# Kernel tuning notes

Hardware: AMD Instinct MI355X
Metric: run time of the kernel (lower is better)

## Reference

```python
import jax, jax.numpy as jnp
import numpy as np

IN_CH = 2048
OUT_CH = 2048
BATCH = 8192


def setup_inputs() -> dict:
    key = jax.random.key(0)
    ks = jax.random.split(key, 8)
    bound = 1.0 / np.sqrt(IN_CH)  # torch nn.Linear default init range
    inp = {
        "input": jax.random.normal(ks[0], (BATCH, IN_CH), dtype=jnp.float32),
        "hidden": jax.random.normal(ks[1], (BATCH, OUT_CH), dtype=jnp.float32),
        "cell": jax.random.normal(ks[2], (BATCH, OUT_CH), dtype=jnp.float32),
        # Fused gate weights: [IN_CH, 4*OUT_CH] for (forget, input, output, state)
        "W": jax.random.uniform(ks[3], (IN_CH, 4 * OUT_CH), minval=-bound, maxval=bound, dtype=jnp.float32),
        "b": jax.random.uniform(ks[4], (4 * OUT_CH,), minval=-bound, maxval=bound, dtype=jnp.float32),
    }
    return inp


def reference(input, hidden, cell, W, b):
    # One fused GEMM for all four gates, then fused elementwise gate math.
    gates = input @ W + b  # [B, 4*OUT_CH]
    f_g, i_g, o_g, s_g = jnp.split(gates, 4, axis=-1)
    # NOTE: original module applies sigmoid (not tanh) to the state gate.
    forget_gate = jax.nn.sigmoid(f_g)
    input_gate = jax.nn.sigmoid(i_g)
    output_gate = jax.nn.sigmoid(o_g)
    state_gate = jax.nn.sigmoid(s_g)
    new_cell = forget_gate * cell + input_gate * state_gate
    new_hidden = output_gate * jnp.tanh(new_cell)
    return (new_hidden, new_cell)
```

## Files before the change

kernel.cpp:

```cpp
#include <hip/hip_runtime.h>
#include <cstddef>
#include <cstdint>

#define B_ROWS 8192
#define K_DIM  2048
#define N_GATE 2048
#define NG     4
#define W_COLS (NG * N_GATE)

#define BM  128
#define BGN 64
#define BK  32
#define KT  (K_DIM / BK)

typedef __attribute__((ext_vector_type(8))) short s16x8;
typedef __attribute__((ext_vector_type(4))) short s16x4;
typedef __attribute__((ext_vector_type(4))) float f32x4;

__device__ __forceinline__ float fast_sigmoid(float x) {
  return 1.0f / (1.0f + __expf(-x));
}
__device__ __forceinline__ float fast_tanh(float x) {
  return 1.0f - 2.0f / (__expf(2.0f * x) + 1.0f);
}

__global__ void convert_in_kernel(const float4* __restrict__ src,
                                  s16x4* __restrict__ dst, int n4) {
  int idx = blockIdx.x * blockDim.x + threadIdx.x;
  int stride = gridDim.x * blockDim.x;
  for (int i = idx; i < n4; i += stride) {
    float4 v = src[i];
    s16x4 o = { __builtin_bit_cast(short, (__bf16)v.x),
                __builtin_bit_cast(short, (__bf16)v.y),
                __builtin_bit_cast(short, (__bf16)v.z),
                __builtin_bit_cast(short, (__bf16)v.w) };
    dst[i] = o;
  }
}

__global__ void convert_w_kernel(const float* __restrict__ W,
                                 short* __restrict__ Wt) {
  __shared__ float tile[32][33];
  int n0 = blockIdx.x * 32;
  int k0 = blockIdx.y * 32;
  int tx = threadIdx.x, ty = threadIdx.y;
#pragma unroll
  for (int j = 0; j < 32; j += 8)
    tile[ty + j][tx] = W[(size_t)(k0 + ty + j) * W_COLS + n0 + tx];
  __syncthreads();
#pragma unroll
  for (int j = 0; j < 32; j += 8)
    Wt[(size_t)(n0 + ty + j) * K_DIM + k0 + tx] =
        __builtin_bit_cast(short, (__bf16)tile[tx][ty + j]);
}

#define GL16(gsrc, ldst)                                                        \
  __builtin_amdgcn_global_load_lds(                                             \
      (const __attribute__((address_space(1))) unsigned int*)(gsrc),            \
      (__attribute__((address_space(3))) unsigned int*)(ldst), 16, 0, 0)

__global__ __launch_bounds__(256, 2) void lstm_gemm_kernel(
    const short* __restrict__ Abf,
    const short* __restrict__ Wt,
    const float* __restrict__ bias,
    const float* __restrict__ cell,
    float* __restrict__ outH,
    float* __restrict__ outC) {
  __shared__ short As[2][BM * BK];
  __shared__ short Bs[2][NG * BGN * BK];

  const int tid = threadIdx.x;
  const int lane = tid & 63;
  const int wid = tid >> 6;
  const int wm = wid >> 1;
  const int wn = wid & 1;
  const int lrow = lane & 15;
  const int lk = lane >> 4;

  const int bid = blockIdx.x;
  const int x = bid & 7;
  const int ii = bid >> 3;
  const int tn = x * 4 + (ii & 3);
  const int tm = ii >> 2;
  const int m0 = tm * BM;
  const int n0 = tn * BGN;

  f32x4 acc[NG][4][2];
#pragma unroll
  for (int g = 0; g < NG; ++g)
#pragma unroll
    for (int mi = 0; mi < 4; ++mi)
#pragma unroll
      for (int ni = 0; ni < 2; ++ni)
        acc[g][mi][ni] = (f32x4){0.f, 0.f, 0.f, 0.f};

  int a_off[4];
#pragma unroll
  for (int mi = 0; mi < 4; ++mi) {
    int ar = wm * 64 + mi * 16 + lrow;
    a_off[mi] = (ar * 4 + (lk ^ ((ar >> 1) & 3))) * 16;
  }
  int b_off[NG][2];
#pragma unroll
  for (int g = 0; g < NG; ++g)
#pragma unroll
    for (int ni = 0; ni < 2; ++ni) {
      int br = wn * 32 + ni * 16 + lrow;
      b_off[g][ni] = (g * 256 + br * 4 + (lk ^ ((br >> 1) & 3))) * 16;
    }

  auto stage = [&](int buf, int kk) {
#pragma unroll
    for (int j = 0; j < 2; ++j) {
      int p = j * 256 + tid;
      int row = p >> 2;
      int gl = (p & 3) ^ ((p >> 3) & 3);
      GL16(Abf + (size_t)(m0 + row) * K_DIM + kk + gl * 8, &As[buf][p * 8]);
    }
#pragma unroll
    for (int g = 0; g < NG; ++g) {
      int row = tid >> 2;
      int gl = (tid & 3) ^ ((tid >> 3) & 3);
      GL16(Wt + (size_t)(g * N_GATE + n0 + row) * K_DIM + kk + gl * 8,
           &Bs[buf][(g * 256 + tid) * 8]);
    }
  };

  stage(0, 0);
  __syncthreads();

  for (int kt = 0; kt < KT; ++kt) {
    const int cur = kt & 1;
    if (kt + 1 < KT) stage(cur ^ 1, (kt + 1) * BK);

    const char* abase = (const char*)As[cur];
    const char* bbase = (const char*)Bs[cur];
    s16x8 af[4];
#pragma unroll
    for (int mi = 0; mi < 4; ++mi)
      af[mi] = *reinterpret_cast<const s16x8*>(abase + a_off[mi]);
#pragma unroll
    for (int g = 0; g < NG; ++g) {
      s16x8 bf0 = *reinterpret_cast<const s16x8*>(bbase + b_off[g][0]);
      s16x8 bf1 = *reinterpret_cast<const s16x8*>(bbase + b_off[g][1]);
#pragma unroll
      for (int mi = 0; mi < 4; ++mi) {
        acc[g][mi][0] = __builtin_amdgcn_mfma_f32_16x16x32_bf16(
            af[mi], bf0, acc[g][mi][0], 0, 0, 0);
        acc[g][mi][1] = __builtin_amdgcn_mfma_f32_16x16x32_bf16(
            af[mi], bf1, acc[g][mi][1], 0, 0, 0);
      }
    }
    __syncthreads();
  }

#pragma unroll
  for (int ni = 0; ni < 2; ++ni) {
    const int n = n0 + wn * 32 + ni * 16 + lrow;
    const float bf_ = bias[n];
    const float bi_ = bias[N_GATE + n];
    const float bo_ = bias[2 * N_GATE + n];
    const float bs_ = bias[3 * N_GATE + n];
#pragma unroll
    for (int mi = 0; mi < 4; ++mi) {
#pragma unroll
      for (int r = 0; r < 4; ++r) {
        const int m = m0 + wm * 64 + mi * 16 + lk * 4 + r;
        const size_t off = (size_t)m * N_GATE + n;
        const float fg = fast_sigmoid(acc[0][mi][ni][r] + bf_);
        const float ig = fast_sigmoid(acc[1][mi][ni][r] + bi_);
        const float og = fast_sigmoid(acc[2][mi][ni][r] + bo_);
        const float sg = fast_sigmoid(acc[3][mi][ni][r] + bs_);
        const float cn = fg * cell[off] + ig * sg;
        outC[off] = cn;
        outH[off] = og * fast_tanh(cn);
      }
    }
  }
}

extern "C" void kernel_launch(void* const* d_in, const int* in_sizes, int n_in,
                              void* d_out, int out_size, void* d_ws, size_t ws_size,
                              hipStream_t stream) {
  const float* inp  = (const float*)d_in[0];
  const float* cell = (const float*)d_in[2];
  const float* W    = (const float*)d_in[3];
  const float* bias = (const float*)d_in[4];

  float* outH = (float*)d_out;
  float* outC = (float*)d_out + (size_t)B_ROWS * N_GATE;

  short* Abf = (short*)d_ws;
  short* Wt  = (short*)d_ws + (size_t)B_ROWS * K_DIM;

  {
    int n4 = (B_ROWS * K_DIM) / 4;
    convert_in_kernel<<<2048, 256, 0, stream>>>((const float4*)inp,
                                                (s16x4*)Abf, n4);
  }
  {
    dim3 grid(W_COLS / 32, K_DIM / 32);
    dim3 block(32, 8);
    convert_w_kernel<<<grid, block, 0, stream>>>(W, Wt);
  }
  {
    int nblocks = (B_ROWS / BM) * (N_GATE / BGN);
    lstm_gemm_kernel<<<nblocks, 256, 0, stream>>>(Abf, Wt, bias, cell,
                                                  outH, outC);
  }
}
```

Before: 609.5 us.

## Rewrite LSTM GEMM with 256x256 tiles, 8 waves, phased staging pipeline

The fused-gate GEMM moves to a 256-row by 64-column-per-gate block with 512 threads and BK=64. It uses 128KB of dynamic LDS with XOR-swizzled layouts and an explicit phased schedule that interleaves global-to-LDS staging with MFMA bursts, using manual vmcnt waits, barriers and setprio. The input conversion now handles 8 elements per thread, and the weight transpose kernel uses 64x64 tiles with packed bf16 pairs and 16-byte stores. The aim is more data reuse per block and better overlap of loads with compute, at the cost of a large LDS footprint, higher register pressure and fragile hand-written synchronisation.

```diff
diff --git a/kernel.cpp b/kernel.cpp
--- a/kernel.cpp
+++ b/kernel.cpp
@@ -8,13 +8,11 @@
 #define NG     4
 #define W_COLS (NG * N_GATE)
 
-#define BM  128
-#define BGN 64
-#define BK  32
-#define KT  (K_DIM / BK)
+#define BM   256
+#define BK   64
+#define NTIL 32
 
 typedef __attribute__((ext_vector_type(8))) short s16x8;
-typedef __attribute__((ext_vector_type(4))) short s16x4;
 typedef __attribute__((ext_vector_type(4))) float f32x4;
 
 __device__ __forceinline__ float fast_sigmoid(float x) {
@@ -25,33 +23,66 @@
 }
 
 __global__ void convert_in_kernel(const float4* __restrict__ src,
-                                  s16x4* __restrict__ dst, int n4) {
+                                  s16x8* __restrict__ dst, int n8) {
   int idx = blockIdx.x * blockDim.x + threadIdx.x;
   int stride = gridDim.x * blockDim.x;
-  for (int i = idx; i < n4; i += stride) {
-    float4 v = src[i];
-    s16x4 o = { __builtin_bit_cast(short, (__bf16)v.x),
-                __builtin_bit_cast(short, (__bf16)v.y),
-                __builtin_bit_cast(short, (__bf16)v.z),
-                __builtin_bit_cast(short, (__bf16)v.w) };
+  for (int i = idx; i < n8; i += stride) {
+    float4 a = src[2 * i], b = src[2 * i + 1];
+    s16x8 o = { __builtin_bit_cast(short, (__bf16)a.x),
+                __builtin_bit_cast(short, (__bf16)a.y),
+                __builtin_bit_cast(short, (__bf16)a.z),
+                __builtin_bit_cast(short, (__bf16)a.w),
+                __builtin_bit_cast(short, (__bf16)b.x),
+                __builtin_bit_cast(short, (__bf16)b.y),
+                __builtin_bit_cast(short, (__bf16)b.z),
+                __builtin_bit_cast(short, (__bf16)b.w) };
     dst[i] = o;
   }
 }
 
-__global__ void convert_w_kernel(const float* __restrict__ W,
-                                 short* __restrict__ Wt) {
-  __shared__ float tile[32][33];
-  int n0 = blockIdx.x * 32;
-  int k0 = blockIdx.y * 32;
-  int tx = threadIdx.x, ty = threadIdx.y;
-#pragma unroll
-  for (int j = 0; j < 32; j += 8)
-    tile[ty + j][tx] = W[(size_t)(k0 + ty + j) * W_COLS + n0 + tx];
+__device__ __forceinline__ unsigned int pack2bf16(float x, float y) {
+  unsigned short lo = __builtin_bit_cast(unsigned short, (__bf16)x);
+  unsigned short hi = __builtin_bit_cast(unsigned short, (__bf16)y);
+  return ((unsigned int)hi << 16) | lo;
+}
+
+__global__ __launch_bounds__(256) void convert_w_kernel(const float* __restrict__ W,
+                                                        short* __restrict__ Wt) {
+  __shared__ unsigned int tile[64 * 32];
+  const int t = threadIdx.x;
+  const int n0 = blockIdx.x * 64;
+  const int k0 = blockIdx.y * 64;
+  {
+    const int kr = t >> 2, seg = t & 3;
+    const float4* src = (const float4*)(W + (size_t)(k0 + kr) * W_COLS + n0 + seg * 16);
+#pragma unroll
+    for (int u = 0; u < 4; ++u) {
+      float4 v = src[u];
+      const int np = seg * 8 + u * 2;
+      tile[kr * 32 + (np ^ (kr & 31))]       = pack2bf16(v.x, v.y);
+      tile[kr * 32 + ((np + 1) ^ (kr & 31))] = pack2bf16(v.z, v.w);
+    }
+  }
   __syncthreads();
-#pragma unroll
-  for (int j = 0; j < 32; j += 8)
-    Wt[(size_t)(n0 + ty + j) * K_DIM + k0 + tx] =
-        __builtin_bit_cast(short, (__bf16)tile[tx][ty + j]);
+  {
+    const int np = t >> 3;
+    const int kb = t & 7;
+    unsigned int w[8];
+#pragma unroll
+    for (int v = 0; v < 8; ++v) {
+      const int k = kb * 8 + v;
+      w[v] = tile[k * 32 + (np ^ (k & 31))];
+    }
+    s16x8 lo, hi;
+#pragma unroll
+    for (int v = 0; v < 8; ++v) {
+      lo[v] = (short)(w[v] & 0xffff);
+      hi[v] = (short)(w[v] >> 16);
+    }
+    short* d0 = Wt + (size_t)(n0 + 2 * np) * K_DIM + k0 + kb * 8;
+    *(s16x8*)d0 = lo;
+    *(s16x8*)(d0 + K_DIM) = hi;
+  }
 }
 
 #define GL16(gsrc, ldst)                                                        \
@@ -59,118 +90,152 @@
       (const __attribute__((address_space(1))) unsigned int*)(gsrc),            \
       (__attribute__((address_space(3))) unsigned int*)(ldst), 16, 0, 0)
 
-__global__ __launch_bounds__(256, 2) void lstm_gemm_kernel(
+#define MFMA16 __builtin_amdgcn_mfma_f32_16x16x32_bf16
+
+__global__ __launch_bounds__(512, 2) void lstm_gemm_kernel(
     const short* __restrict__ Abf,
     const short* __restrict__ Wt,
     const float* __restrict__ bias,
     const float* __restrict__ cell,
     float* __restrict__ outH,
     float* __restrict__ outC) {
-  __shared__ short As[2][BM * BK];
-  __shared__ short Bs[2][NG * BGN * BK];
+  extern __shared__ short lds[];
 
   const int tid = threadIdx.x;
   const int lane = tid & 63;
   const int wid = tid >> 6;
-  const int wm = wid >> 1;
-  const int wn = wid & 1;
+  const int wm = wid >> 2;
+  const int wn = wid & 3;
   const int lrow = lane & 15;
   const int lk = lane >> 4;
 
   const int bid = blockIdx.x;
-  const int x = bid & 7;
-  const int ii = bid >> 3;
-  const int tn = x * 4 + (ii & 3);
-  const int tm = ii >> 2;
+  const int xcd = bid & 7, j = bid >> 3;
+  const int tn = xcd * 4 + (j >> 5);
+  const int tm = j & 31;
   const int m0 = tm * BM;
-  const int n0 = tn * BGN;
-
-  f32x4 acc[NG][4][2];
-#pragma unroll
-  for (int g = 0; g < NG; ++g)
-#pragma unroll
-    for (int mi = 0; mi < 4; ++mi)
-#pragma unroll
-      for (int ni = 0; ni < 2; ++ni)
-        acc[g][mi][ni] = (f32x4){0.f, 0.f, 0.f, 0.f};
-
-  int a_off[4];
-#pragma unroll
-  for (int mi = 0; mi < 4; ++mi) {
-    int ar = wm * 64 + mi * 16 + lrow;
-    a_off[mi] = (ar * 4 + (lk ^ ((ar >> 1) & 3))) * 16;
-  }
-  int b_off[NG][2];
-#pragma unroll
-  for (int g = 0; g < NG; ++g)
-#pragma unroll
-    for (int ni = 0; ni < 2; ++ni) {
-      int br = wn * 32 + ni * 16 + lrow;
-      b_off[g][ni] = (g * 256 + br * 4 + (lk ^ ((br >> 1) & 3))) * 16;
-    }
-
-  auto stage = [&](int buf, int kk) {
-#pragma unroll
-    for (int j = 0; j < 2; ++j) {
-      int p = j * 256 + tid;
-      int row = p >> 2;
-      int gl = (p & 3) ^ ((p >> 3) & 3);
-      GL16(Abf + (size_t)(m0 + row) * K_DIM + kk + gl * 8, &As[buf][p * 8]);
-    }
-#pragma unroll
-    for (int g = 0; g < NG; ++g) {
-      int row = tid >> 2;
-      int gl = (tid & 3) ^ ((tid >> 3) & 3);
-      GL16(Wt + (size_t)(g * N_GATE + n0 + row) * K_DIM + kk + gl * 8,
-           &Bs[buf][(g * 256 + tid) * 8]);
-    }
-  };
-
-  stage(0, 0);
-  __syncthreads();
-
-  for (int kt = 0; kt < KT; ++kt) {
-    const int cur = kt & 1;
-    if (kt + 1 < KT) stage(cur ^ 1, (kt + 1) * BK);
-
-    const char* abase = (const char*)As[cur];
-    const char* bbase = (const char*)Bs[cur];
-    s16x8 af[4];
-#pragma unroll
-    for (int mi = 0; mi < 4; ++mi)
-      af[mi] = *reinterpret_cast<const s16x8*>(abase + a_off[mi]);
-#pragma unroll
-    for (int g = 0; g < NG; ++g) {
-      s16x8 bf0 = *reinterpret_cast<const s16x8*>(bbase + b_off[g][0]);
-      s16x8 bf1 = *reinterpret_cast<const s16x8*>(bbase + b_off[g][1]);
-#pragma unroll
-      for (int mi = 0; mi < 4; ++mi) {
-        acc[g][mi][0] = __builtin_amdgcn_mfma_f32_16x16x32_bf16(
-            af[mi], bf0, acc[g][mi][0], 0, 0, 0);
-        acc[g][mi][1] = __builtin_amdgcn_mfma_f32_16x16x32_bf16(
-            af[mi], bf1, acc[g][mi][1], 0, 0, 0);
-      }
-    }
-    __syncthreads();
-  }
-
-#pragma unroll
-  for (int ni = 0; ni < 2; ++ni) {
-    const int n = n0 + wn * 32 + ni * 16 + lrow;
-    const float bf_ = bias[n];
-    const float bi_ = bias[N_GATE + n];
-    const float bo_ = bias[2 * N_GATE + n];
-    const float bs_ = bias[3 * N_GATE + n];
-#pragma unroll
-    for (int mi = 0; mi < 4; ++mi) {
+  const int n0 = tn * 64;
+
+  size_t a_src[2][2], b_src[2][2];
+#pragma unroll
+  for (int h = 0; h < 2; ++h)
+#pragma unroll
+    for (int jj = 0; jj < 2; ++jj) {
+      const int p = h * 1024 + jj * 512 + tid;
+      const int r = p >> 3;
+      const int gl = (p & 7) ^ (r & 7);
+      a_src[h][jj] = (size_t)(m0 + r) * K_DIM + gl * 8;
+      const int wn16 = r >> 6, g = (r >> 4) & 3, nc4 = r & 15;
+      b_src[h][jj] = (size_t)(g * N_GATE + n0 + wn16 * 16 + nc4) * K_DIM + gl * 8;
+    }
+
+#define STAGE_A(BUF, H, KT) do {                                                 \
+    GL16(Abf + a_src[H][0] + (size_t)(KT) * BK,                                  \
+         lds + (BUF) * 16384 + ((H) * 1024 + tid) * 8);                          \
+    GL16(Abf + a_src[H][1] + (size_t)(KT) * BK,                                  \
+         lds + (BUF) * 16384 + ((H) * 1024 + 512 + tid) * 8);                    \
+  } while (0)
+#define STAGE_B(BUF, H, KT) do {                                                 \
+    GL16(Wt + b_src[H][0] + (size_t)(KT) * BK,                                   \
+         lds + 32768 + (BUF) * 16384 + ((H) * 1024 + tid) * 8);                  \
+    GL16(Wt + b_src[H][1] + (size_t)(KT) * BK,                                   \
+         lds + 32768 + (BUF) * 16384 + ((H) * 1024 + 512 + tid) * 8);            \
+  } while (0)
+
+  const int pg0 = (lk ^ (lrow & 7)) * 16;
+  const int pg1 = ((4 + lk) ^ (lrow & 7)) * 16;
+  const char* aK0 = (const char*)lds + (wm * 128 + lrow) * 128 + pg0;
+  const char* aK1 = (const char*)lds + (wm * 128 + lrow) * 128 + pg1;
+  const char* bK0 = (const char*)lds + 65536 + (wn * 64 + lrow) * 128 + pg0;
+  const char* bK1 = (const char*)lds + 65536 + (wn * 64 + lrow) * 128 + pg1;
+#define AF(BUF, MI, KK) (*(const s16x8*)(aK##KK + (BUF) * 32768 + (MI) * 2048))
+#define BFR(BUF, G, KK) (*(const s16x8*)(bK##KK + (BUF) * 32768 + (G) * 2048))
+
+  f32x4 acc[8][4];
+#pragma unroll
+  for (int mi = 0; mi < 8; ++mi)
+#pragma unroll
+    for (int g = 0; g < 4; ++g) acc[mi][g] = (f32x4){0.f, 0.f, 0.f, 0.f};
+
+  s16x8 bfr[4][2];
+
+#define MMQ(MI, A0, A1) do {                                                     \
+    acc[MI][0] = MFMA16(A0, bfr[0][0], acc[MI][0], 0, 0, 0);                     \
+    acc[MI][0] = MFMA16(A1, bfr[0][1], acc[MI][0], 0, 0, 0);                     \
+    acc[MI][1] = MFMA16(A0, bfr[1][0], acc[MI][1], 0, 0, 0);                     \
+    acc[MI][1] = MFMA16(A1, bfr[1][1], acc[MI][1], 0, 0, 0);                     \
+    acc[MI][2] = MFMA16(A0, bfr[2][0], acc[MI][2], 0, 0, 0);                     \
+    acc[MI][2] = MFMA16(A1, bfr[2][1], acc[MI][2], 0, 0, 0);                     \
+    acc[MI][3] = MFMA16(A0, bfr[3][0], acc[MI][3], 0, 0, 0);                     \
+    acc[MI][3] = MFMA16(A1, bfr[3][1], acc[MI][3], 0, 0, 0);                     \
+  } while (0)
+
+#define VM_NONE do {} while (0)
+#define VM_4 asm volatile("s_waitcnt vmcnt(4)" ::: "memory")
+#define VM_0 asm volatile("s_waitcnt vmcnt(0)" ::: "memory")
+
+#define PHASE(BUF, Q, LOADB, STG, VM) do {                                       \
+    if (LOADB) {                                                                 \
+      bfr[0][0] = BFR(BUF, 0, 0); bfr[0][1] = BFR(BUF, 0, 1);                    \
+      bfr[1][0] = BFR(BUF, 1, 0); bfr[1][1] = BFR(BUF, 1, 1);                    \
+      bfr[2][0] = BFR(BUF, 2, 0); bfr[2][1] = BFR(BUF, 2, 1);                    \
+      bfr[3][0] = BFR(BUF, 3, 0); bfr[3][1] = BFR(BUF, 3, 1);                    \
+    }                                                                            \
+    s16x8 af00 = AF(BUF, 2 * (Q), 0), af01 = AF(BUF, 2 * (Q), 1);                \
+    s16x8 af10 = AF(BUF, 2 * (Q) + 1, 0), af11 = AF(BUF, 2 * (Q) + 1, 1);        \
+    STG;                                                                         \
+    VM;                                                                          \
+    __builtin_amdgcn_s_barrier();                                                \
+    asm volatile("s_waitcnt lgkmcnt(0)" ::: "memory");                           \
+    __builtin_amdgcn_s_setprio(1);                                               \
+    MMQ(2 * (Q), af00, af01);                                                    \
+    MMQ(2 * (Q) + 1, af10, af11);                                                \
+    __builtin_amdgcn_s_setprio(0);                                               \
+    __builtin_amdgcn_s_barrier();                                                \
+  } while (0)
+
+  STAGE_B(0, 0, 0); STAGE_B(0, 1, 0); STAGE_A(0, 0, 0); STAGE_A(0, 1, 0);
+  STAGE_B(1, 0, 1); STAGE_B(1, 1, 1);
+  VM_4;
+  __builtin_amdgcn_s_barrier();
+
+  for (int i = 0; i < NTIL / 2 - 1; ++i) {
+    const int t1 = 2 * i + 1, t2 = 2 * i + 2, t3 = 2 * i + 3;
+    PHASE(0, 0, 1, { STAGE_A(1, 0, t1); }, VM_NONE);
+    PHASE(0, 1, 0, { STAGE_A(1, 1, t1); }, VM_NONE);
+    PHASE(0, 2, 0, { STAGE_B(0, 0, t2); }, VM_NONE);
+    PHASE(0, 3, 0, { STAGE_B(0, 1, t2); }, VM_4);
+    PHASE(1, 0, 1, { STAGE_A(0, 0, t2); }, VM_NONE);
+    PHASE(1, 1, 0, { STAGE_A(0, 1, t2); }, VM_NONE);
+    PHASE(1, 2, 0, { STAGE_B(1, 0, t3); }, VM_NONE);
+    PHASE(1, 3, 0, { STAGE_B(1, 1, t3); }, VM_4);
+  }
+
+  PHASE(0, 0, 1, { STAGE_A(1, 0, 31); }, VM_NONE);
+  PHASE(0, 1, 0, { STAGE_A(1, 1, 31); }, VM_NONE);
+  PHASE(0, 2, 0, {}, VM_NONE);
+  PHASE(0, 3, 0, {}, VM_0);
+  PHASE(1, 0, 1, {}, VM_NONE);
+  PHASE(1, 1, 0, {}, VM_NONE);
+  PHASE(1, 2, 0, {}, VM_NONE);
+  PHASE(1, 3, 0, {}, VM_NONE);
+
+  {
+    const int n = n0 + wn * 16 + lrow;
+    const float b0 = bias[n];
+    const float b1 = bias[N_GATE + n];
+    const float b2 = bias[2 * N_GATE + n];
+    const float b3 = bias[3 * N_GATE + n];
+    const size_t base = (size_t)(m0 + wm * 128 + lk * 4) * N_GATE + n;
+#pragma unroll
+    for (int mi = 0; mi < 8; ++mi) {
 #pragma unroll
       for (int r = 0; r < 4; ++r) {
-        const int m = m0 + wm * 64 + mi * 16 + lk * 4 + r;
-        const size_t off = (size_t)m * N_GATE + n;
-        const float fg = fast_sigmoid(acc[0][mi][ni][r] + bf_);
-        const float ig = fast_sigmoid(acc[1][mi][ni][r] + bi_);
-        const float og = fast_sigmoid(acc[2][mi][ni][r] + bo_);
-        const float sg = fast_sigmoid(acc[3][mi][ni][r] + bs_);
+        const size_t off = base + (size_t)(mi * 16 + r) * N_GATE;
+        const float fg = fast_sigmoid(acc[mi][0][r] + b0);
+        const float ig = fast_sigmoid(acc[mi][1][r] + b1);
+        const float og = fast_sigmoid(acc[mi][2][r] + b2);
+        const float sg = fast_sigmoid(acc[mi][3][r] + b3);
         const float cn = fg * cell[off] + ig * sg;
         outC[off] = cn;
         outH[off] = og * fast_tanh(cn);
@@ -194,18 +259,19 @@
   short* Wt  = (short*)d_ws + (size_t)B_ROWS * K_DIM;
 
   {
-    int n4 = (B_ROWS * K_DIM) / 4;
+    int n8 = (B_ROWS * K_DIM) / 8;
     convert_in_kernel<<<2048, 256, 0, stream>>>((const float4*)inp,
-                                                (s16x4*)Abf, n4);
-  }
-  {
-    dim3 grid(W_COLS / 32, K_DIM / 32);
-    dim3 block(32, 8);
-    convert_w_kernel<<<grid, block, 0, stream>>>(W, Wt);
-  }
-  {
-    int nblocks = (B_ROWS / BM) * (N_GATE / BGN);
-    lstm_gemm_kernel<<<nblocks, 256, 0, stream>>>(Abf, Wt, bias, cell,
-                                                  outH, outC);
-  }
-}
+                                                (s16x8*)Abf, n8);
+  }
+  {
+    dim3 grid(W_COLS / 64, K_DIM / 64);
+    convert_w_kernel<<<grid, 256, 0, stream>>>(W, Wt);
+  }
+  {
+    (void)hipFuncSetAttribute(reinterpret_cast<const void*>(&lstm_gemm_kernel),
+                              hipFuncAttributeMaxDynamicSharedMemorySize, 131072);
+    int nblocks = (B_ROWS / BM) * (N_GATE / 64);
+    lstm_gemm_kernel<<<nblocks, 512, 131072, stream>>>(Abf, Wt, bias, cell,
+                                                       outH, outC);
+  }
+}
```

After: 536.8 us. 11.9% less time.
